# Optimization experiments

Hardware: AMD Instinct MI355X
Metric: run time of the kernel (lower is better)

Reference implementation:

```python
import jax, jax.numpy as jnp
import numpy as np

N_NODES = 100000
N_EDGES = 1200000
IN_DIM, HIDDEN, OUT_DIM = 128, 64, 64


def setup_inputs() -> dict:
    key = jax.random.key(0)
    k1, k2, k3, k4 = jax.random.split(key, 4)
    x = jax.random.normal(k1, (N_NODES, IN_DIM), dtype=jnp.float32)
    edge_index = jax.random.randint(k2, (2, N_EDGES), 0, N_NODES, dtype=jnp.int64)
    # Glorot-style init for GCNConv linear weights (PyG uses glorot), zero bias.
    W1 = jax.random.normal(k3, (IN_DIM, HIDDEN), dtype=jnp.float32) * np.float32(np.sqrt(2.0 / (IN_DIM + HIDDEN)))
    b1 = jnp.zeros((HIDDEN,), dtype=jnp.float32)
    W2 = jax.random.normal(k4, (HIDDEN, OUT_DIM), dtype=jnp.float32) * np.float32(np.sqrt(2.0 / (HIDDEN + OUT_DIM)))
    b2 = jnp.zeros((OUT_DIM,), dtype=jnp.float32)
    return {"x": x, "edge_index": edge_index, "W1": W1, "b1": b1, "W2": W2, "b2": b2}


def _gcn_conv(h, src, dst, deg_inv_sqrt, W, b):
    # PyG GCNConv: out = scatter_add( norm * (h @ W)[src] -> dst ) + b
    n = h.shape[0]
    norm = deg_inv_sqrt[src] * deg_inv_sqrt[dst]            # [E+N]
    hw = h @ W                                              # [N, F_out]
    msg = hw[src] * norm[:, None]                           # [E+N, F_out] gather
    out = jnp.zeros((n, W.shape[1]), h.dtype).at[dst].add(msg)  # scatter-add
    return out + b


def reference(x, edge_index, W1, b1, W2, b2):
    n = x.shape[0]
    # Add self-loops (GCNConv default add_self_loops=True).
    loop = jnp.arange(n, dtype=edge_index.dtype)
    src = jnp.concatenate([edge_index[0], loop])  # source nodes
    dst = jnp.concatenate([edge_index[1], loop])  # target nodes (aggregation)
    # Symmetric normalization D^{-1/2} (A+I) D^{-1/2}; degree at targets.
    deg = jnp.zeros((n,), x.dtype).at[dst].add(jnp.ones((), x.dtype))
    deg_inv_sqrt = jnp.where(deg > 0, jax.lax.rsqrt(deg), 0.0)
    h = _gcn_conv(x, src, dst, deg_inv_sqrt, W1, b1)
    h = jax.nn.relu(h)
    h = _gcn_conv(h, src, dst, deg_inv_sqrt, W2, b2)
    h = jax.nn.relu(h)
    return h
```

## Files before the change

kernel.cpp:

```cpp
#include <hip/hip_runtime.h>
#include <hip/hip_fp16.h>
#include <cstdint>
#include <cstddef>

#define NN 100000
#define NE 1200000
#define NBKT 1563
#define CAP_B 2048
#define PBLK 256
#define PCHK ((NE + PBLK - 1) / PBLK)

typedef _Float16 f16x8 __attribute__((ext_vector_type(8)));
typedef float f32x4 __attribute__((ext_vector_type(4)));

__global__ __launch_bounds__(256) void partition_hier(
    const int* __restrict__ ei, int* __restrict__ cur,
    unsigned* __restrict__ recs, unsigned* __restrict__ ovfn,
    uint2* __restrict__ ovf, int E) {
    __shared__ int hist[NBKT];
    __shared__ int base[NBKT];
    const int tid = threadIdx.x;
    for (int i = tid; i < NBKT; i += 256) hist[i] = 0;
    __syncthreads();
    const int lo = blockIdx.x * PCHK, hi = min(lo + PCHK, E);
    for (int e = lo + tid; e < hi; e += 256)
        atomicAdd(&hist[ei[E + e] >> 6], 1);
    __syncthreads();
    for (int i = tid; i < NBKT; i += 256) {
        int c = hist[i];
        base[i] = c ? atomicAdd(&cur[i], c) : 0;
        hist[i] = 0;
    }
    __syncthreads();
    for (int e = lo + tid; e < hi; e += 256) {
        int d = ei[E + e];
        int s = ei[e];
        int b = d >> 6;
        int lp = atomicAdd(&hist[b], 1);
        int pos = base[b] + lp;
        if (pos < CAP_B)
            recs[(size_t)b * CAP_B + pos] = ((unsigned)s << 6) | (unsigned)(d & 63);
        else {
            unsigned o = atomicAdd(ovfn, 1);
            if (o < 4096) ovf[o] = make_uint2((unsigned)s, (unsigned)d);
        }
    }
}

__global__ __launch_bounds__(256) void bucket_dis(
    const int* __restrict__ cur, const unsigned* __restrict__ recs,
    const unsigned* __restrict__ ovfn, const uint2* __restrict__ ovf,
    float* __restrict__ dis, int n) {
    __shared__ int cnt[64];
    const int b = blockIdx.x, tid = threadIdx.x;
    if (tid < 64) cnt[tid] = 0;
    __syncthreads();
    int c = min(cur[b], CAP_B);
    const unsigned* st = recs + (size_t)b * CAP_B;
    for (int i = tid; i < c; i += 256) atomicAdd(&cnt[st[i] & 63], 1);
    __syncthreads();
    if (tid < 64) {
        int g = b * 64 + tid;
        if (g < n) {
            int cc = cnt[tid];
            unsigned no = *ovfn;
            for (unsigned i = 0; i < no; i++)
                if ((int)ovf[i].y == g) cc++;
            dis[g] = rsqrtf((float)cc + 1.0f);
        }
    }
}

__global__ __launch_bounds__(256) void agg_bucket3(
    const int* __restrict__ cur, const unsigned* __restrict__ recs,
    const __half* __restrict__ hw, const float* __restrict__ dis,
    const float* __restrict__ bias, float* __restrict__ out,
    const unsigned* __restrict__ ovfn, const uint2* __restrict__ ovf, int n) {
    __shared__ unsigned srec[CAP_B];
    __shared__ int cnt[64], off[65], woff[64], pfx[64];
    __shared__ float disD[64];
    const int b = blockIdx.x, tid = threadIdx.x;
    if (tid < 64) {
        cnt[tid] = 0;
        int g = b * 64 + tid;
        disD[tid] = (g < n) ? dis[g] : 0.f;
    }
    __syncthreads();

    const int c = min(cur[b], CAP_B);
    const unsigned* st = recs + (size_t)b * CAP_B;
    for (int i = tid; i < c; i += 256) atomicAdd(&cnt[st[i] & 63], 1);
    __syncthreads();
    if (tid < 64) pfx[tid] = cnt[tid];
    __syncthreads();
    for (int s = 1; s < 64; s <<= 1) {
        int v = (tid < 64 && tid >= s) ? pfx[tid - s] : 0;
        __syncthreads();
        if (tid < 64) pfx[tid] += v;
        __syncthreads();
    }
    if (tid == 0) off[0] = 0;
    if (tid < 64) { off[tid + 1] = pfx[tid]; woff[tid] = pfx[tid] - cnt[tid]; }
    __syncthreads();
    for (int i = tid; i < c; i += 256) {
        unsigned k = st[i];
        int p = atomicAdd(&woff[k & 63], 1);
        srec[p] = k;
    }
    __syncthreads();

    const uint2* hwq = (const uint2*)hw;
    const int slot = tid >> 4, sub = tid & 15;
    const unsigned no = *ovfn;
    const float4 bb = ((const float4*)bias)[sub];

#define LD1(q) { float2 g01 = __half22float2(*(__half2*)&(q).x); \
                 float2 g23 = __half22float2(*(__half2*)&(q).y); \
                 a0 += g01.x; a1 += g01.y; a2 += g23.x; a3 += g23.y; }

    for (int j = 0; j < 4; j++) {
        int nl = slot * 4 + j;
        int g = b * 64 + nl;
        if (g >= n) break;
        uint2 qs = hwq[(size_t)g * 16 + sub];
        float a0 = 0.f, a1 = 0.f, a2 = 0.f, a3 = 0.f;
        LD1(qs);

        int e = off[nl], end = off[nl + 1];
        for (; e + 8 <= end; e += 8) {
            uint2 q0 = hwq[(size_t)(srec[e + 0] >> 6) * 16 + sub];
            uint2 q1 = hwq[(size_t)(srec[e + 1] >> 6) * 16 + sub];
            uint2 q2 = hwq[(size_t)(srec[e + 2] >> 6) * 16 + sub];
            uint2 q3 = hwq[(size_t)(srec[e + 3] >> 6) * 16 + sub];
            uint2 q4 = hwq[(size_t)(srec[e + 4] >> 6) * 16 + sub];
            uint2 q5 = hwq[(size_t)(srec[e + 5] >> 6) * 16 + sub];
            uint2 q6 = hwq[(size_t)(srec[e + 6] >> 6) * 16 + sub];
            uint2 q7 = hwq[(size_t)(srec[e + 7] >> 6) * 16 + sub];
            LD1(q0); LD1(q1); LD1(q2); LD1(q3);
            LD1(q4); LD1(q5); LD1(q6); LD1(q7);
        }
        for (; e + 4 <= end; e += 4) {
            uint2 q0 = hwq[(size_t)(srec[e + 0] >> 6) * 16 + sub];
            uint2 q1 = hwq[(size_t)(srec[e + 1] >> 6) * 16 + sub];
            uint2 q2 = hwq[(size_t)(srec[e + 2] >> 6) * 16 + sub];
            uint2 q3 = hwq[(size_t)(srec[e + 3] >> 6) * 16 + sub];
            LD1(q0); LD1(q1); LD1(q2); LD1(q3);
        }
        for (; e < end; e++) {
            uint2 q = hwq[(size_t)(srec[e] >> 6) * 16 + sub];
            LD1(q);
        }
        for (unsigned i = 0; i < no; i++) {
            uint2 o = ovf[i];
            if ((int)o.y == g) { uint2 q = hwq[(size_t)o.x * 16 + sub]; LD1(q); }
        }
        float di = disD[nl];
        float4 oo;
        oo.x = fmaf(di, a0, bb.x);
        oo.y = fmaf(di, a1, bb.y);
        oo.z = fmaf(di, a2, bb.z);
        oo.w = fmaf(di, a3, bb.w);
        oo.x = oo.x > 0.f ? oo.x : 0.f;
        oo.y = oo.y > 0.f ? oo.y : 0.f;
        oo.z = oo.z > 0.f ? oo.z : 0.f;
        oo.w = oo.w > 0.f ? oo.w : 0.f;
        ((float4*)out)[(size_t)g * 16 + sub] = oo;
    }
#undef LD1
}

template <int K>
__global__ __launch_bounds__(256) void gemm_mfma(const float* __restrict__ A,
                                                 const float* __restrict__ W,
                                                 const float* __restrict__ dis,
                                                 __half* __restrict__ C, int n) {
    constexpr int KB = K / 32;
    __shared__ f16x8 sAf[4 * KB * 64];
    __shared__ f16x8 sWf[4 * KB * 64];
    __shared__ float sdis[64];
    const int tid = threadIdx.x;
    const int row0 = blockIdx.x * 64;

    if (tid < 64) {
        int rw = row0 + tid;
        sdis[tid] = (rw < n) ? dis[rw] : 0.f;
    }

    _Float16* sAh = (_Float16*)sAf;
    const float4* A4 = (const float4*)A;
#pragma unroll
    for (int it = 0; it < K / 16; ++it) {
        int f = it * 256 + tid;
        int row = f / (K / 4);
        int kq = f % (K / 4);
        int k0 = kq * 4;
        float4 a;
        if (row0 + row < n) a = A4[(size_t)(row0 + row) * (K / 4) + kq];
        else { a.x = 0.f; a.y = 0.f; a.z = 0.f; a.w = 0.f; }
        int rt = row >> 4;
        int kb = k0 >> 5;
        int lane = (row & 15) | (((k0 >> 3) & 3) << 4);
        int base = ((rt * KB + kb) * 64 + lane) * 8 + (k0 & 7);
        sAh[base + 0] = (_Float16)a.x;
        sAh[base + 1] = (_Float16)a.y;
        sAh[base + 2] = (_Float16)a.z;
        sAh[base + 3] = (_Float16)a.w;
    }
    _Float16* sWh = (_Float16*)sWf;
    {
        int nn = tid & 63;
        int ct = nn >> 4;
        int lbase = nn & 15;
        for (int k = tid >> 6; k < K; k += 4) {
            float w = W[(size_t)k * 64 + nn];
            int kb = k >> 5;
            int lane = lbase | (((k >> 3) & 3) << 4);
            sWh[((ct * KB + kb) * 64 + lane) * 8 + (k & 7)] = (_Float16)w;
        }
    }
    __syncthreads();

    const int wv = tid >> 6;
    const int lane = tid & 63;
    f32x4 acc[4];
#pragma unroll
    for (int rt = 0; rt < 4; ++rt) acc[rt] = (f32x4){0.f, 0.f, 0.f, 0.f};

#pragma unroll
    for (int kb = 0; kb < KB; ++kb) {
        f16x8 bf = sWf[(wv * KB + kb) * 64 + lane];
#pragma unroll
        for (int rt = 0; rt < 4; ++rt) {
            f16x8 af = sAf[(rt * KB + kb) * 64 + lane];
            acc[rt] = __builtin_amdgcn_mfma_f32_16x16x32_f16(af, bf, acc[rt], 0, 0, 0);
        }
    }

    int col = wv * 16 + (lane & 15);
    int rbase = (lane >> 4) * 4;
#pragma unroll
    for (int rt = 0; rt < 4; ++rt) {
#pragma unroll
        for (int r = 0; r < 4; ++r) {
            int row = row0 + rt * 16 + rbase + r;
            if (row < n)
                C[(size_t)row * 64 + col] = __float2half(acc[rt][r] * sdis[rt * 16 + rbase + r]);
        }
    }
}

__global__ void fill_kernel(float* __restrict__ p, float v, int n) {
    int i = blockIdx.x * blockDim.x + threadIdx.x;
    if (i < n) p[i] = v;
}
__global__ void degree_kernel(const int* __restrict__ ei, float* __restrict__ deg, int E) {
    int stride = gridDim.x * blockDim.x;
    for (int e = blockIdx.x * blockDim.x + threadIdx.x; e < E; e += stride)
        atomicAdd(&deg[ei[E + e]], 1.0f);
}
__global__ void rsqrt_kernel(float* __restrict__ deg, int n) {
    int i = blockIdx.x * blockDim.x + threadIdx.x;
    if (i < n) deg[i] = rsqrtf(deg[i]);
}
template <int K>
__global__ __launch_bounds__(256) void gemm_tile(const float* __restrict__ A,
                                                 const float* __restrict__ W,
                                                 float* __restrict__ C, int n) {
    __shared__ float sA[64 * K];
    __shared__ float sW[K * 64];
    const int tid = threadIdx.x;
    const int row0 = blockIdx.x * 64;
    const int rows = min(64, n - row0);
    const float4* W4 = (const float4*)W;
    float4* sW4 = (float4*)sW;
    for (int i = tid; i < K * 16; i += 256) sW4[i] = W4[i];
    const float4* A4 = (const float4*)(A + (size_t)row0 * K);
    float4* sA4 = (float4*)sA;
    const int nElem = rows * (K / 4);
    for (int i = tid; i < nElem; i += 256) sA4[i] = A4[i];
    __syncthreads();
    const int col = tid & 63;
    const int ty  = tid >> 6;
    float acc[16];
#pragma unroll
    for (int r = 0; r < 16; r++) acc[r] = 0.f;
    for (int k = 0; k < K; k += 4) {
        float w0 = sW[(k + 0) * 64 + col];
        float w1 = sW[(k + 1) * 64 + col];
        float w2 = sW[(k + 2) * 64 + col];
        float w3 = sW[(k + 3) * 64 + col];
#pragma unroll
        for (int r = 0; r < 16; r++) {
            const float4 a = *(const float4*)&sA[(ty + 4 * r) * K + k];
            acc[r] = fmaf(a.x, w0, acc[r]);
            acc[r] = fmaf(a.y, w1, acc[r]);
            acc[r] = fmaf(a.z, w2, acc[r]);
            acc[r] = fmaf(a.w, w3, acc[r]);
        }
    }
#pragma unroll
    for (int r = 0; r < 16; r++) {
        int row = ty + 4 * r;
        if (row < rows) C[(size_t)(row0 + row) * 64 + col] = acc[r];
    }
}
__global__ void scatter_kernel(const int* __restrict__ ei, const float* __restrict__ hw,
                               const float* __restrict__ dis, float* __restrict__ agg, int E) {
    int gtid = blockIdx.x * blockDim.x + threadIdx.x;
    int wave = gtid >> 6, lane = threadIdx.x & 63;
    int nwaves = (gridDim.x * blockDim.x) >> 6;
    for (int e = wave; e < E; e += nwaves) {
        int s = ei[e], d = ei[E + e];
        float v = hw[(size_t)s * 64 + lane] * dis[s] * dis[d];
        atomicAdd(&agg[(size_t)d * 64 + lane], v);
    }
}
__global__ void finalize_kernel(float* __restrict__ agg, const float* __restrict__ hw,
                                const float* __restrict__ dis, const float* __restrict__ b, int n) {
    int i = blockIdx.x * blockDim.x + threadIdx.x;
    if (i < n * 64) {
        int node = i >> 6, col = i & 63;
        float di = dis[node];
        float v = agg[i] + hw[i] * di * di + b[col];
        agg[i] = v > 0.0f ? v : 0.0f;
    }
}

extern "C" void kernel_launch(void* const* d_in, const int* in_sizes, int n_in,
                              void* d_out, int out_size, void* d_ws, size_t ws_size,
                              hipStream_t stream) {
    const float* x  = (const float*)d_in[0];
    const int*   ei = (const int*)d_in[1];
    const float* W1 = (const float*)d_in[2];
    const float* b1 = (const float*)d_in[3];
    const float* W2 = (const float*)d_in[4];
    const float* b2 = (const float*)d_in[5];
    float* out = (float*)d_out;

    const int N = NN, E = NE;
    char* ws = (char*)d_ws;
    const int gemmGrid = (N + 63) / 64;

    if (ws_size >= 38200000u) {
        float*    dis  = (float*)ws;
        int*      cur  = (int*)(ws + (1u << 19));
        unsigned* ovfn = (unsigned*)(ws + 589824u);
        uint2*    ovf  = (uint2*)(ws + 593920u);
        unsigned* recs = (unsigned*)(ws + (1u << 20));
        __half*   hwa  = (__half*)(ws + 14680064u);

        hipMemsetAsync(cur, 0, NBKT * sizeof(int), stream);
        hipMemsetAsync(ovfn, 0, sizeof(unsigned), stream);
        partition_hier<<<PBLK, 256, 0, stream>>>(ei, cur, recs, ovfn, ovf, E);
        bucket_dis<<<NBKT, 256, 0, stream>>>(cur, recs, ovfn, ovf, dis, N);

        gemm_mfma<128><<<gemmGrid, 256, 0, stream>>>(x, W1, dis, hwa, N);
        agg_bucket3<<<NBKT, 256, 0, stream>>>(cur, recs, hwa, dis, b1, out, ovfn, ovf, N);
        gemm_mfma<64><<<gemmGrid, 256, 0, stream>>>(out, W2, dis, hwa, N);
        agg_bucket3<<<NBKT, 256, 0, stream>>>(cur, recs, hwa, dis, b2, out, ovfn, ovf, N);
    } else {
        float* dis  = (float*)ws;
        float* bufA = (float*)(ws + (1 << 19));
        const size_t featBytes = (size_t)N * 64 * sizeof(float);

        fill_kernel<<<(N + 255) / 256, 256, 0, stream>>>(dis, 1.0f, N);
        degree_kernel<<<2048, 256, 0, stream>>>(ei, dis, E);
        rsqrt_kernel<<<(N + 255) / 256, 256, 0, stream>>>(dis, N);

        gemm_tile<128><<<gemmGrid, 256, 0, stream>>>(x, W1, bufA, N);
        hipMemsetAsync(out, 0, featBytes, stream);
        scatter_kernel<<<2048, 256, 0, stream>>>(ei, bufA, dis, out, E);
        finalize_kernel<<<(N * 64 + 255) / 256, 256, 0, stream>>>(out, bufA, dis, b1, N);

        gemm_tile<64><<<gemmGrid, 256, 0, stream>>>(out, W2, bufA, N);
        hipMemsetAsync(out, 0, featBytes, stream);
        scatter_kernel<<<2048, 256, 0, stream>>>(ei, bufA, dis, out, E);
        finalize_kernel<<<(N * 64 + 255) / 256, 256, 0, stream>>>(out, bufA, dis, b2, N);
    }
}
```

Before: 129.5 us.

## Store layer-1 output in fp16, add half-input GEMM, shrink bucket capacity

The first aggregation now writes its ReLU output as packed fp16 into a separate buffer, and a new fp16-input MFMA GEMM reads it for layer 2. This halves the intermediate write and the next read. Separately, the two memsets become one tiny zero kernel, the per-bucket record capacity drops from 2048 to 1536, and partition uses 128 blocks instead of 256. The smaller capacity means more edges spill to the overflow list, which every block scans linearly. It also lowers the precision of the intermediate activations.

```diff
diff --git a/kernel.cpp b/kernel.cpp
--- a/kernel.cpp
+++ b/kernel.cpp
@@ -6,12 +6,18 @@
 #define NN 100000
 #define NE 1200000
 #define NBKT 1563
-#define CAP_B 2048
-#define PBLK 256
+#define CAP_B 1536
+#define PBLK 128
 #define PCHK ((NE + PBLK - 1) / PBLK)
 
 typedef _Float16 f16x8 __attribute__((ext_vector_type(8)));
 typedef float f32x4 __attribute__((ext_vector_type(4)));
+
+__global__ void zero_kernel(int* __restrict__ cur, unsigned* __restrict__ ovfn) {
+    int i = blockIdx.x * blockDim.x + threadIdx.x;
+    if (i < NBKT) cur[i] = 0;
+    if (i == NBKT) *ovfn = 0;
+}
 
 __global__ __launch_bounds__(256) void partition_hier(
     const int* __restrict__ ei, int* __restrict__ cur,
@@ -71,10 +77,11 @@
     }
 }
 
+template <bool HALF_OUT>
 __global__ __launch_bounds__(256) void agg_bucket3(
     const int* __restrict__ cur, const unsigned* __restrict__ recs,
     const __half* __restrict__ hw, const float* __restrict__ dis,
-    const float* __restrict__ bias, float* __restrict__ out,
+    const float* __restrict__ bias, void* __restrict__ outv,
     const unsigned* __restrict__ ovfn, const uint2* __restrict__ ovf, int n) {
     __shared__ unsigned srec[CAP_B];
     __shared__ int cnt[64], off[65], woff[64], pfx[64];
@@ -155,16 +162,25 @@
             if ((int)o.y == g) { uint2 q = hwq[(size_t)o.x * 16 + sub]; LD1(q); }
         }
         float di = disD[nl];
-        float4 oo;
-        oo.x = fmaf(di, a0, bb.x);
-        oo.y = fmaf(di, a1, bb.y);
-        oo.z = fmaf(di, a2, bb.z);
-        oo.w = fmaf(di, a3, bb.w);
-        oo.x = oo.x > 0.f ? oo.x : 0.f;
-        oo.y = oo.y > 0.f ? oo.y : 0.f;
-        oo.z = oo.z > 0.f ? oo.z : 0.f;
-        oo.w = oo.w > 0.f ? oo.w : 0.f;
-        ((float4*)out)[(size_t)g * 16 + sub] = oo;
+        float o0 = fmaf(di, a0, bb.x);
+        float o1 = fmaf(di, a1, bb.y);
+        float o2 = fmaf(di, a2, bb.z);
+        float o3 = fmaf(di, a3, bb.w);
+        o0 = o0 > 0.f ? o0 : 0.f;
+        o1 = o1 > 0.f ? o1 : 0.f;
+        o2 = o2 > 0.f ? o2 : 0.f;
+        o3 = o3 > 0.f ? o3 : 0.f;
+        if (HALF_OUT) {
+            __half2 p01 = __floats2half2_rn(o0, o1);
+            __half2 p23 = __floats2half2_rn(o2, o3);
+            uint2 pk;
+            pk.x = *(unsigned*)&p01;
+            pk.y = *(unsigned*)&p23;
+            ((uint2*)outv)[(size_t)g * 16 + sub] = pk;
+        } else {
+            float4 oo; oo.x = o0; oo.y = o1; oo.z = o2; oo.w = o3;
+            ((float4*)outv)[(size_t)g * 16 + sub] = oo;
+        }
     }
 #undef LD1
 }
@@ -249,6 +265,86 @@
     }
 }
 
+__global__ __launch_bounds__(256) void gemm_mfma_h(const __half* __restrict__ A,
+                                                   const float* __restrict__ W,
+                                                   const float* __restrict__ dis,
+                                                   __half* __restrict__ C, int n) {
+    constexpr int K = 64, KB = 2;
+    __shared__ f16x8 sAf[4 * KB * 64];
+    __shared__ f16x8 sWf[4 * KB * 64];
+    __shared__ float sdis[64];
+    const int tid = threadIdx.x;
+    const int row0 = blockIdx.x * 64;
+
+    if (tid < 64) {
+        int rw = row0 + tid;
+        sdis[tid] = (rw < n) ? dis[rw] : 0.f;
+    }
+
+    _Float16* sAh = (_Float16*)sAf;
+    const uint2* A2 = (const uint2*)A;
+#pragma unroll
+    for (int it = 0; it < 4; ++it) {
+        int f = it * 256 + tid;
+        int row = f >> 4;
+        int kq = f & 15;
+        int k0 = kq * 4;
+        uint2 a;
+        if (row0 + row < n) a = A2[(size_t)(row0 + row) * 16 + kq];
+        else { a.x = 0u; a.y = 0u; }
+        _Float16* ap = (_Float16*)&a;
+        int rt = row >> 4;
+        int kb = k0 >> 5;
+        int lane = (row & 15) | (((k0 >> 3) & 3) << 4);
+        int base = ((rt * KB + kb) * 64 + lane) * 8 + (k0 & 7);
+        sAh[base + 0] = ap[0];
+        sAh[base + 1] = ap[1];
+        sAh[base + 2] = ap[2];
+        sAh[base + 3] = ap[3];
+    }
+    _Float16* sWh = (_Float16*)sWf;
+    {
+        int nn = tid & 63;
+        int ct = nn >> 4;
+        int lbase = nn & 15;
+        for (int k = tid >> 6; k < K; k += 4) {
+            float w = W[(size_t)k * 64 + nn];
+            int kb = k >> 5;
+            int lane = lbase | (((k >> 3) & 3) << 4);
+            sWh[((ct * KB + kb) * 64 + lane) * 8 + (k & 7)] = (_Float16)w;
+        }
+    }
+    __syncthreads();
+
+    const int wv = tid >> 6;
+    const int lane = tid & 63;
+    f32x4 acc[4];
+#pragma unroll
+    for (int rt = 0; rt < 4; ++rt) acc[rt] = (f32x4){0.f, 0.f, 0.f, 0.f};
+
+#pragma unroll
+    for (int kb = 0; kb < KB; ++kb) {
+        f16x8 bf = sWf[(wv * KB + kb) * 64 + lane];
+#pragma unroll
+        for (int rt = 0; rt < 4; ++rt) {
+            f16x8 af = sAf[(rt * KB + kb) * 64 + lane];
+            acc[rt] = __builtin_amdgcn_mfma_f32_16x16x32_f16(af, bf, acc[rt], 0, 0, 0);
+        }
+    }
+
+    int col = wv * 16 + (lane & 15);
+    int rbase = (lane >> 4) * 4;
+#pragma unroll
+    for (int rt = 0; rt < 4; ++rt) {
+#pragma unroll
+        for (int r = 0; r < 4; ++r) {
+            int row = row0 + rt * 16 + rbase + r;
+            if (row < n)
+                C[(size_t)row * 64 + col] = __float2half(acc[rt][r] * sdis[rt * 16 + rbase + r]);
+        }
+    }
+}
+
 __global__ void fill_kernel(float* __restrict__ p, float v, int n) {
     int i = blockIdx.x * blockDim.x + threadIdx.x;
     if (i < n) p[i] = v;
@@ -347,17 +443,17 @@
         unsigned* ovfn = (unsigned*)(ws + 589824u);
         uint2*    ovf  = (uint2*)(ws + 593920u);
         unsigned* recs = (unsigned*)(ws + (1u << 20));
-        __half*   hwa  = (__half*)(ws + 14680064u);
-
-        hipMemsetAsync(cur, 0, NBKT * sizeof(int), stream);
-        hipMemsetAsync(ovfn, 0, sizeof(unsigned), stream);
+        __half*   hwa  = (__half*)(ws + 11534336u);
+        __half*   hvb  = (__half*)(ws + 25165824u);
+
+        zero_kernel<<<(NBKT + 256) / 256, 256, 0, stream>>>(cur, ovfn);
         partition_hier<<<PBLK, 256, 0, stream>>>(ei, cur, recs, ovfn, ovf, E);
         bucket_dis<<<NBKT, 256, 0, stream>>>(cur, recs, ovfn, ovf, dis, N);
 
         gemm_mfma<128><<<gemmGrid, 256, 0, stream>>>(x, W1, dis, hwa, N);
-        agg_bucket3<<<NBKT, 256, 0, stream>>>(cur, recs, hwa, dis, b1, out, ovfn, ovf, N);
-        gemm_mfma<64><<<gemmGrid, 256, 0, stream>>>(out, W2, dis, hwa, N);
-        agg_bucket3<<<NBKT, 256, 0, stream>>>(cur, recs, hwa, dis, b2, out, ovfn, ovf, N);
+        agg_bucket3<true><<<NBKT, 256, 0, stream>>>(cur, recs, hwa, dis, b1, hvb, ovfn, ovf, N);
+        gemm_mfma_h<<<gemmGrid, 256, 0, stream>>>(hvb, W2, dis, hwa, N);
+        agg_bucket3<false><<<NBKT, 256, 0, stream>>>(cur, recs, hwa, dis, b2, out, ovfn, ovf, N);
     } else {
         float* dis  = (float*)ws;
         float* bufA = (float*)(ws + (1 << 19));
```

Result: no change. 130.5 us (+0.8%).
